# Optimization experiments

Measured on AMD Instinct MI355X. Metric: run time of the kernel, lower is better.

The kernel has to match this reference:

```python
import jax, jax.numpy as jnp
import numpy as np

OUT_FEATURES = 4096
IN_FEATURES = 4096
GROUP_SIZE = 128
NUM_GROUPS = OUT_FEATURES // GROUP_SIZE  # groups along output-channel axis (axis=0)


def _unpack_int8_to_int4(packed, num_elements):
    # Each int8 byte holds two signed int4 values: low nibble first, then high nibble.
    p = packed.astype(jnp.int8)
    low = jnp.right_shift(jnp.left_shift(p, 4), 4)   # sign-extended low nibble, in [-8, 7]
    high = jnp.right_shift(p, 4)                      # arithmetic shift -> sign-extended high nibble
    vals = jnp.stack([low, high], axis=-1).reshape(-1)
    return vals[:num_elements]


def _dequantize_weight(packed_weight, scales, zero_points):
    int4 = _unpack_int8_to_int4(packed_weight, OUT_FEATURES * IN_FEATURES)
    w = int4.astype(jnp.float32).reshape(NUM_GROUPS, GROUP_SIZE, IN_FEATURES)
    # per-group (over output channels): (q - zp) * scale
    w = (w - zero_points[:, None, None]) * scales[:, None, None]
    return w.reshape(OUT_FEATURES, IN_FEATURES)


def setup_inputs() -> dict:
    key = jax.random.key(0)
    k_x, k_w, k_s, k_zp, k_b = jax.random.split(key, 5)
    x = jax.random.normal(k_x, (8192, IN_FEATURES), dtype=jnp.float32)
    # packed int4 weights stored as signed bytes
    packed_weight = jax.random.randint(k_w, (OUT_FEATURES * IN_FEATURES // 2,), 0, 256, dtype=jnp.int32) - 128
    scales = jax.random.uniform(k_s, (NUM_GROUPS,), dtype=jnp.float32) * 0.02 + 0.001
    zero_points = jax.random.normal(k_zp, (NUM_GROUPS,), dtype=jnp.float32) * 0.5
    bias = jax.random.normal(k_b, (OUT_FEATURES,), dtype=jnp.float32)
    return {"x": x, "packed_weight": packed_weight, "scales": scales,
            "zero_points": zero_points, "bias": bias}


def reference(x, packed_weight, scales, zero_points, bias):
    weight = _dequantize_weight(packed_weight, scales, zero_points)  # [out, in]
    return jnp.einsum('bi,oi->bo', x, weight) + bias
```

## Files before the change

kernel.cpp:

```cpp
#include <hip/hip_runtime.h>
#include <cstdint>
#include <cstddef>

#define M_DIM 8192
#define N_DIM 4096
#define K_DIM 4096
#define CHUNK_M 4096

typedef __attribute__((ext_vector_type(8))) short bf16x8;
typedef __attribute__((ext_vector_type(4))) float floatx4;

__device__ __forceinline__ ushort f2bf_rne(float f) {
    union { float f; uint32_t u; } a;
    a.f = f;
    uint32_t u = a.u;
    uint32_t r = (u + 0x7fffu + ((u >> 16) & 1u)) >> 16;
    return (ushort)r;
}

__device__ __forceinline__ uint32_t pk_bf_trunc(float f0, float f1) {
    return __builtin_amdgcn_perm(__float_as_uint(f1), __float_as_uint(f0),
                                 0x07060302u);
}

__global__ void dequant_w_kernel(const int4* __restrict__ pw,
                                 const float* __restrict__ scales,
                                 const float* __restrict__ zps,
                                 uint4* __restrict__ wb, int np4) {
    int p4 = blockIdx.x * blockDim.x + threadIdx.x;
    if (p4 >= np4) return;
    int p = p4 * 4;
    int g = p >> 18;
    float s = scales[g];
    float b = -zps[g] * s;
    int4 v = pw[p4];
    int vv[4] = { v.x, v.y, v.z, v.w };
    ushort o[8];
#pragma unroll
    for (int j = 0; j < 4; ++j) {
        int lo = ((int)((uint32_t)vv[j] << 28)) >> 28;
        int hi = ((int)((uint32_t)vv[j] << 24)) >> 28;
        o[2 * j]     = f2bf_rne(fmaf((float)lo, s, b));
        o[2 * j + 1] = f2bf_rne(fmaf((float)hi, s, b));
    }
    uint4 st;
    st.x = (uint32_t)o[0] | ((uint32_t)o[1] << 16);
    st.y = (uint32_t)o[2] | ((uint32_t)o[3] << 16);
    st.z = (uint32_t)o[4] | ((uint32_t)o[5] << 16);
    st.w = (uint32_t)o[6] | ((uint32_t)o[7] << 16);
    wb[p4] = st;
}

__global__ void convert_x_kernel(const float4* __restrict__ x4,
                                 ushort4* __restrict__ out4, int n4) {
    int i = blockIdx.x * blockDim.x + threadIdx.x;
    if (i >= n4) return;
    float4 v = x4[i];
    ushort4 o;
    o.x = f2bf_rne(v.x);
    o.y = f2bf_rne(v.y);
    o.z = f2bf_rne(v.z);
    o.w = f2bf_rne(v.w);
    out4[i] = o;
}

#define BM 128
#define BN 128
#define BK 32

__global__ void gemm_bf16_kernel(const ushort* __restrict__ A,
                                 const ushort* __restrict__ B,
                                 const float* __restrict__ bias,
                                 float* __restrict__ C) {
    __shared__ ushort As[BM * BK];
    __shared__ ushort Bs[BN * BK];

    const int tid  = threadIdx.x;
    const int lane = tid & 63;
    const int wave = tid >> 6;
    const int wm   = wave >> 1;
    const int wn   = wave & 1;
    const int bm   = blockIdx.y;
    const int bn   = blockIdx.x;

    const int scol = (lane & 3) * 8;
    const ushort* Ab = A + (size_t)(bm * BM) * K_DIM;
    const ushort* Bb = B + (size_t)(bn * BN) * K_DIM;

    floatx4 acc[4][4] = {};

    for (int k0 = 0; k0 < K_DIM; k0 += BK) {
#pragma unroll
        for (int q = 0; q < 2; ++q) {
            const int chunk = wave * 2 + q;
            const int r = chunk * 16 + (lane >> 2);
            const ushort* ga = Ab + (size_t)r * K_DIM + k0 + scol;
            const ushort* gb = Bb + (size_t)r * K_DIM + k0 + scol;
            __builtin_amdgcn_global_load_lds(
                (const __attribute__((address_space(1))) void*)ga,
                (__attribute__((address_space(3))) void*)(As + chunk * 512),
                16, 0, 0);
            __builtin_amdgcn_global_load_lds(
                (const __attribute__((address_space(1))) void*)gb,
                (__attribute__((address_space(3))) void*)(Bs + chunk * 512),
                16, 0, 0);
        }
        __syncthreads();

        bf16x8 af[4], bfr[4];
        const int frow = lane & 15;
        const int fcol = (lane >> 4) * 8;
#pragma unroll
        for (int i = 0; i < 4; ++i) {
            af[i]  = *(const bf16x8*)(As + (wm * 64 + i * 16 + frow) * BK + fcol);
            bfr[i] = *(const bf16x8*)(Bs + (wn * 64 + i * 16 + frow) * BK + fcol);
        }
#pragma unroll
        for (int i = 0; i < 4; ++i)
#pragma unroll
            for (int j = 0; j < 4; ++j)
                acc[i][j] = __builtin_amdgcn_mfma_f32_16x16x32_bf16(
                    af[i], bfr[j], acc[i][j], 0, 0, 0);
        __syncthreads();
    }

    const int crow0 = bm * BM + wm * 64;
    const int ccol0 = bn * BN + wn * 64;
    const int rl = lane >> 4;
    const int cl = lane & 15;
#pragma unroll
    for (int j = 0; j < 4; ++j) {
        const int col = ccol0 + j * 16 + cl;
        const float bv = bias[col];
#pragma unroll
        for (int i = 0; i < 4; ++i) {
            const int row = crow0 + i * 16 + rl * 4;
            float* cp = C + (size_t)row * N_DIM + col;
#pragma unroll
            for (int r = 0; r < 4; ++r)
                cp[(size_t)r * N_DIM] = acc[i][j][r] + bv;
        }
    }
}

__global__ void gemm_fused_kernel(const float* __restrict__ X,
                                  const ushort* __restrict__ B,
                                  const float* __restrict__ bias,
                                  float* __restrict__ C) {
    __shared__ ushort As[BM * BK];
    __shared__ ushort Bs[BN * BK];

    const int tid  = threadIdx.x;
    const int lane = tid & 63;
    const int wave = tid >> 6;
    const int wm   = wave >> 1;
    const int wn   = wave & 1;
    const int bm   = blockIdx.y;
    const int bn   = blockIdx.x;

    const int ar = tid >> 2;
    const int ac = (tid & 3) * 8;
    const float* xp0 = X + (size_t)(bm * BM + ar) * K_DIM + ac;
    const float* xp1 = xp0 + (size_t)64 * K_DIM;
    ushort* as0 = As + ar * BK + ac;
    ushort* as1 = as0 + 64 * BK;

    const int scol = (lane & 3) * 8;
    const ushort* Bb = B + (size_t)(bn * BN) * K_DIM;

    floatx4 acc[4][4] = {};

    for (int k0 = 0; k0 < K_DIM; k0 += BK) {
        float4 a0 = *(const float4*)(xp0 + k0);
        float4 a1 = *(const float4*)(xp0 + k0 + 4);
        float4 b0 = *(const float4*)(xp1 + k0);
        float4 b1 = *(const float4*)(xp1 + k0 + 4);
#pragma unroll
        for (int q = 0; q < 2; ++q) {
            const int chunk = wave * 2 + q;
            const int r = chunk * 16 + (lane >> 2);
            const ushort* gb = Bb + (size_t)r * K_DIM + k0 + scol;
            __builtin_amdgcn_global_load_lds(
                (const __attribute__((address_space(1))) void*)gb,
                (__attribute__((address_space(3))) void*)(Bs + chunk * 512),
                16, 0, 0);
        }
        uint4 w0, w1;
        w0.x = pk_bf_trunc(a0.x, a0.y);
        w0.y = pk_bf_trunc(a0.z, a0.w);
        w0.z = pk_bf_trunc(a1.x, a1.y);
        w0.w = pk_bf_trunc(a1.z, a1.w);
        w1.x = pk_bf_trunc(b0.x, b0.y);
        w1.y = pk_bf_trunc(b0.z, b0.w);
        w1.z = pk_bf_trunc(b1.x, b1.y);
        w1.w = pk_bf_trunc(b1.z, b1.w);
        *(uint4*)as0 = w0;
        *(uint4*)as1 = w1;

        __syncthreads();

        bf16x8 af[4], bfr[4];
        const int frow = lane & 15;
        const int fcol = (lane >> 4) * 8;
#pragma unroll
        for (int i = 0; i < 4; ++i) {
            af[i]  = *(const bf16x8*)(As + (wm * 64 + i * 16 + frow) * BK + fcol);
            bfr[i] = *(const bf16x8*)(Bs + (wn * 64 + i * 16 + frow) * BK + fcol);
        }
#pragma unroll
        for (int i = 0; i < 4; ++i)
#pragma unroll
            for (int j = 0; j < 4; ++j)
                acc[i][j] = __builtin_amdgcn_mfma_f32_16x16x32_bf16(
                    af[i], bfr[j], acc[i][j], 0, 0, 0);
        __syncthreads();
    }

    const int crow0 = bm * BM + wm * 64;
    const int ccol0 = bn * BN + wn * 64;
    const int rl = lane >> 4;
    const int cl = lane & 15;
#pragma unroll
    for (int j = 0; j < 4; ++j) {
        const int col = ccol0 + j * 16 + cl;
        const float bv = bias[col];
#pragma unroll
        for (int i = 0; i < 4; ++i) {
            const int row = crow0 + i * 16 + rl * 4;
            float* cp = C + (size_t)row * N_DIM + col;
#pragma unroll
            for (int r = 0; r < 4; ++r)
                cp[(size_t)r * N_DIM] = acc[i][j][r] + bv;
        }
    }
}

extern "C" void kernel_launch(void* const* d_in, const int* in_sizes, int n_in,
                              void* d_out, int out_size, void* d_ws, size_t ws_size,
                              hipStream_t stream) {
    const float* x      = (const float*)d_in[0];
    const int*   pw     = (const int*)d_in[1];
    const float* scales = (const float*)d_in[2];
    const float* zps    = (const float*)d_in[3];
    const float* bias   = (const float*)d_in[4];
    float* out = (float*)d_out;

    ushort* wb = (ushort*)d_ws;

    {
        int np4 = (N_DIM * K_DIM / 2) / 4;
        dequant_w_kernel<<<np4 / 256, 256, 0, stream>>>(
            (const int4*)pw, scales, zps, (uint4*)wb, np4);
    }

    const size_t need = ((size_t)N_DIM * K_DIM + (size_t)CHUNK_M * K_DIM) * 2;
    if (ws_size >= need) {
        ushort* xb = wb + (size_t)N_DIM * K_DIM;
        for (int c = 0; c < M_DIM / CHUNK_M; ++c) {
            const float* xc = x + (size_t)c * CHUNK_M * K_DIM;
            float* oc = out + (size_t)c * CHUNK_M * N_DIM;
            int n4 = (CHUNK_M * K_DIM) / 4;
            convert_x_kernel<<<n4 / 256, 256, 0, stream>>>(
                (const float4*)xc, (ushort4*)xb, n4);
            dim3 grid(N_DIM / BN, CHUNK_M / BM);
            gemm_bf16_kernel<<<grid, 256, 0, stream>>>(xb, wb, bias, oc);
        }
    } else {
        dim3 grid(N_DIM / BN, M_DIM / BM);
        gemm_fused_kernel<<<grid, 256, 0, stream>>>(x, wb, bias, out);
    }
}
```

Measured before the change: 552.1 us.

## Replace 128x128 bf16 GEMM with 256x256 four-stage pipelined kernel

Replaces the simple single-buffered 128x128 GEMM with a 256x256-tile, 512-thread kernel that prefetches three k-tiles ahead into a four-slot LDS ring using global_load_lds. Each iteration is split into two half-steps that interleave A and B staging with MFMA work, and uses barriers, s_setprio and waitcnt to overlap loads with compute. It also swizzles block IDs across 8 groups to improve L2 locality. The larger tile raises per-block data reuse, at the cost of 128KB LDS per block, high register pressure and fragile manual synchronisation.

```diff
diff --git a/kernel.cpp b/kernel.cpp
--- a/kernel.cpp
+++ b/kernel.cpp
@@ -64,84 +64,150 @@
     out4[i] = o;
 }
 
+#define TBM 256
+#define TBN 256
+#define TBK 32
+#define NT  (K_DIM / TBK)
+#define A_E 8192
+#define SLOT_E 16384
+
+__global__ __launch_bounds__(512, 2)
+void gemm_bf16_256(const ushort* __restrict__ A,
+                   const ushort* __restrict__ B,
+                   const float* __restrict__ bias,
+                   float* __restrict__ C) {
+    __shared__ ushort lds[4 * SLOT_E];
+
+    const int tid  = threadIdx.x;
+    const int lane = tid & 63;
+    const int wave = tid >> 6;
+    const int wm   = wave >> 2;
+    const int wn   = wave & 3;
+
+    const int nwg = gridDim.x;
+    const int cpx = nwg >> 3;
+    const int bid = blockIdx.x;
+    const int swz = (bid & 7) * cpx + (bid >> 3);
+    const int bn  = swz & (N_DIM / TBN - 1);
+    const int bm  = swz / (N_DIM / TBN);
+
+    const ushort* Ab = A + (size_t)(bm * TBM) * K_DIM;
+    const ushort* Bb = B + (size_t)(bn * TBN) * K_DIM;
+
+    const int srow = tid >> 2;
+    const int scol = (tid & 3) * 8;
+    const ushort* gA0 = Ab + (size_t)srow * K_DIM + scol;
+    const ushort* gA1 = gA0 + (size_t)128 * K_DIM;
+    const ushort* gB0 = Bb + (size_t)srow * K_DIM + scol;
+    const ushort* gB1 = gB0 + (size_t)128 * K_DIM;
+    const int wdst = wave * 512;
+
+    const int frow = lane & 15;
+    const int fcol = (lane >> 4) * 8;
+    const int aoff = (wm * 128 + frow) * TBK + fcol;
+    const int boff = A_E + (wn * 64 + frow) * TBK + fcol;
+
+    floatx4 acc[8][4] = {};
+
+#define STAGE_A(tt)                                                           \
+    {                                                                          \
+        const int k0s = ((tt) & (NT - 1)) * TBK;                               \
+        ushort* d = lds + ((tt) & 3) * SLOT_E + wdst;                          \
+        __builtin_amdgcn_global_load_lds(                                      \
+            (const __attribute__((address_space(1))) void*)(gA0 + k0s),        \
+            (__attribute__((address_space(3))) void*)d, 16, 0, 0);             \
+        __builtin_amdgcn_global_load_lds(                                      \
+            (const __attribute__((address_space(1))) void*)(gA1 + k0s),        \
+            (__attribute__((address_space(3))) void*)(d + 4096), 16, 0, 0);    \
+    }
+#define STAGE_B(tt)                                                           \
+    {                                                                          \
+        const int k0s = ((tt) & (NT - 1)) * TBK;                               \
+        ushort* d = lds + ((tt) & 3) * SLOT_E + A_E + wdst;                    \
+        __builtin_amdgcn_global_load_lds(                                      \
+            (const __attribute__((address_space(1))) void*)(gB0 + k0s),        \
+            (__attribute__((address_space(3))) void*)d, 16, 0, 0);             \
+        __builtin_amdgcn_global_load_lds(                                      \
+            (const __attribute__((address_space(1))) void*)(gB1 + k0s),        \
+            (__attribute__((address_space(3))) void*)(d + 4096), 16, 0, 0);    \
+    }
+
+    STAGE_A(0) STAGE_B(0)
+    STAGE_A(1) STAGE_B(1)
+    STAGE_A(2) STAGE_B(2)
+    asm volatile("s_waitcnt vmcnt(8)" ::: "memory");
+    __builtin_amdgcn_s_barrier();
+    __builtin_amdgcn_sched_barrier(0);
+
+    for (int t = 0; t < NT; ++t) {
+        const ushort* base = lds + (t & 3) * SLOT_E;
+
+        bf16x8 bf[4], af[4];
+#pragma unroll
+        for (int j = 0; j < 4; ++j)
+            bf[j] = *(const bf16x8*)(base + boff + j * 512);
+#pragma unroll
+        for (int i = 0; i < 4; ++i)
+            af[i] = *(const bf16x8*)(base + aoff + i * 512);
+        STAGE_A(t + 3)
+        __builtin_amdgcn_s_barrier();
+        asm volatile("s_waitcnt lgkmcnt(0)" ::: "memory");
+        __builtin_amdgcn_sched_barrier(0);
+        __builtin_amdgcn_s_setprio(1);
+#pragma unroll
+        for (int i = 0; i < 4; ++i)
+#pragma unroll
+            for (int j = 0; j < 4; ++j)
+                acc[i][j] = __builtin_amdgcn_mfma_f32_16x16x32_bf16(
+                    af[i], bf[j], acc[i][j], 0, 0, 0);
+        __builtin_amdgcn_s_setprio(0);
+        __builtin_amdgcn_s_barrier();
+        __builtin_amdgcn_sched_barrier(0);
+
+#pragma unroll
+        for (int i = 0; i < 4; ++i)
+            af[i] = *(const bf16x8*)(base + aoff + (4 + i) * 512);
+        STAGE_B(t + 3)
+        __builtin_amdgcn_s_barrier();
+        asm volatile("s_waitcnt lgkmcnt(0)" ::: "memory");
+        __builtin_amdgcn_sched_barrier(0);
+        __builtin_amdgcn_s_setprio(1);
+#pragma unroll
+        for (int i = 0; i < 4; ++i)
+#pragma unroll
+            for (int j = 0; j < 4; ++j)
+                acc[4 + i][j] = __builtin_amdgcn_mfma_f32_16x16x32_bf16(
+                    af[i], bf[j], acc[4 + i][j], 0, 0, 0);
+        __builtin_amdgcn_s_setprio(0);
+        asm volatile("s_waitcnt vmcnt(8)" ::: "memory");
+        __builtin_amdgcn_s_barrier();
+        __builtin_amdgcn_sched_barrier(0);
+    }
+#undef STAGE_A
+#undef STAGE_B
+
+    const int crow0 = bm * TBM + wm * 128;
+    const int ccol0 = bn * TBN + wn * 64;
+    const int rl = lane >> 4;
+    const int cl = lane & 15;
+#pragma unroll
+    for (int j = 0; j < 4; ++j) {
+        const int col = ccol0 + j * 16 + cl;
+        const float bv = bias[col];
+#pragma unroll
+        for (int i = 0; i < 8; ++i) {
+            const int row = crow0 + i * 16 + rl * 4;
+            float* cp = C + (size_t)row * N_DIM + col;
+#pragma unroll
+            for (int r = 0; r < 4; ++r)
+                cp[(size_t)r * N_DIM] = acc[i][j][r] + bv;
+        }
+    }
+}
+
 #define BM 128
 #define BN 128
 #define BK 32
-
-__global__ void gemm_bf16_kernel(const ushort* __restrict__ A,
-                                 const ushort* __restrict__ B,
-                                 const float* __restrict__ bias,
-                                 float* __restrict__ C) {
-    __shared__ ushort As[BM * BK];
-    __shared__ ushort Bs[BN * BK];
-
-    const int tid  = threadIdx.x;
-    const int lane = tid & 63;
-    const int wave = tid >> 6;
-    const int wm   = wave >> 1;
-    const int wn   = wave & 1;
-    const int bm   = blockIdx.y;
-    const int bn   = blockIdx.x;
-
-    const int scol = (lane & 3) * 8;
-    const ushort* Ab = A + (size_t)(bm * BM) * K_DIM;
-    const ushort* Bb = B + (size_t)(bn * BN) * K_DIM;
-
-    floatx4 acc[4][4] = {};
-
-    for (int k0 = 0; k0 < K_DIM; k0 += BK) {
-#pragma unroll
-        for (int q = 0; q < 2; ++q) {
-            const int chunk = wave * 2 + q;
-            const int r = chunk * 16 + (lane >> 2);
-            const ushort* ga = Ab + (size_t)r * K_DIM + k0 + scol;
-            const ushort* gb = Bb + (size_t)r * K_DIM + k0 + scol;
-            __builtin_amdgcn_global_load_lds(
-                (const __attribute__((address_space(1))) void*)ga,
-                (__attribute__((address_space(3))) void*)(As + chunk * 512),
-                16, 0, 0);
-            __builtin_amdgcn_global_load_lds(
-                (const __attribute__((address_space(1))) void*)gb,
-                (__attribute__((address_space(3))) void*)(Bs + chunk * 512),
-                16, 0, 0);
-        }
-        __syncthreads();
-
-        bf16x8 af[4], bfr[4];
-        const int frow = lane & 15;
-        const int fcol = (lane >> 4) * 8;
-#pragma unroll
-        for (int i = 0; i < 4; ++i) {
-            af[i]  = *(const bf16x8*)(As + (wm * 64 + i * 16 + frow) * BK + fcol);
-            bfr[i] = *(const bf16x8*)(Bs + (wn * 64 + i * 16 + frow) * BK + fcol);
-        }
-#pragma unroll
-        for (int i = 0; i < 4; ++i)
-#pragma unroll
-            for (int j = 0; j < 4; ++j)
-                acc[i][j] = __builtin_amdgcn_mfma_f32_16x16x32_bf16(
-                    af[i], bfr[j], acc[i][j], 0, 0, 0);
-        __syncthreads();
-    }
-
-    const int crow0 = bm * BM + wm * 64;
-    const int ccol0 = bn * BN + wn * 64;
-    const int rl = lane >> 4;
-    const int cl = lane & 15;
-#pragma unroll
-    for (int j = 0; j < 4; ++j) {
-        const int col = ccol0 + j * 16 + cl;
-        const float bv = bias[col];
-#pragma unroll
-        for (int i = 0; i < 4; ++i) {
-            const int row = crow0 + i * 16 + rl * 4;
-            float* cp = C + (size_t)row * N_DIM + col;
-#pragma unroll
-            for (int r = 0; r < 4; ++r)
-                cp[(size_t)r * N_DIM] = acc[i][j][r] + bv;
-        }
-    }
-}
 
 __global__ void gemm_fused_kernel(const float* __restrict__ X,
                                   const ushort* __restrict__ B,
@@ -262,8 +328,8 @@
             int n4 = (CHUNK_M * K_DIM) / 4;
             convert_x_kernel<<<n4 / 256, 256, 0, stream>>>(
                 (const float4*)xc, (ushort4*)xb, n4);
-            dim3 grid(N_DIM / BN, CHUNK_M / BM);
-            gemm_bf16_kernel<<<grid, 256, 0, stream>>>(xb, wb, bias, oc);
+            int nblk = (CHUNK_M / TBM) * (N_DIM / TBN);
+            gemm_bf16_256<<<nblk, 512, 0, stream>>>(xb, wb, bias, oc);
         }
     } else {
         dim3 grid(N_DIM / BN, M_DIM / BM);
```

Result: faster. 507.9 us (-8.0%).
